# Kernel tuning notes

Hardware: AMD Instinct MI355X
Metric: run time of the kernel (lower is better)

## Reference

```python
import jax, jax.numpy as jnp
import numpy as np

PAD_ID = 0


def setup_inputs() -> dict:
    key = jax.random.key(0)
    ks = jax.random.split(key, 14)
    B, S, T = 64, 128, 32
    E = H = 512
    V = 32000
    s = 0.02
    return {
        "trg_tokens": jax.random.randint(ks[0], (B, T), 0, V),
        "src_tokens": jax.random.randint(ks[1], (B, S), 0, V),
        "encoder_out": jax.random.normal(ks[2], (S, B, 2 * H), jnp.float32),
        "hidden": jax.random.normal(ks[3], (B, H), jnp.float32),
        "embed_w": jax.random.normal(ks[4], (V, E), jnp.float32) * s,
        "attn_W": jax.random.normal(ks[5], (H, 2 * H + H), jnp.float32) * s,
        "attn_b": jnp.zeros((H,), jnp.float32),
        "v": jax.random.uniform(ks[6], (H,), jnp.float32),
        "W_ih": jax.random.normal(ks[7], (3 * H, 2 * H + E), jnp.float32) * s,
        "W_hh": jax.random.normal(ks[8], (3 * H, H), jnp.float32) * s,
        "b_ih": jnp.zeros((3 * H,), jnp.float32),
        "b_hh": jnp.zeros((3 * H,), jnp.float32),
        "out_W": jax.random.normal(ks[9], (V, 2 * H + H + E), jnp.float32) * s,
        "out_b": jnp.zeros((V,), jnp.float32),
    }


def reference(trg_tokens, src_tokens, encoder_out, hidden, embed_w, attn_W,
              attn_b, v, W_ih, W_hh, b_ih, b_hh, out_W, out_b):
    # trg_tokens: [B, T], src_tokens: [B, S] (transposed inside, as in torch)
    B, T = trg_tokens.shape
    S = src_tokens.shape[1]
    H = hidden.shape[1]
    V = out_W.shape[0]

    # Embedding with padding_idx -> zero row at PAD_ID
    emb = embed_w.at[PAD_ID].set(0.0)
    mask = (src_tokens != PAD_ID)              # [B, S]
    enc_bt = jnp.transpose(encoder_out, (1, 0, 2))  # [B, S, 2H]
    trg = trg_tokens.T                          # [T, B]

    def step(h, tok):
        x = emb[tok]                            # [B, E]
        # Bahdanau attention
        hrep = jnp.broadcast_to(h[:, None, :], (B, S, H))
        feat = jnp.concatenate([hrep, enc_bt], axis=2)      # [B, S, H+2H]
        energy = jnp.tanh(feat @ attn_W.T + attn_b)          # [B, S, H]
        scores = jnp.einsum('bsd,d->bs', energy, v)          # [B, S]
        scores = jnp.where(mask, scores, -jnp.inf)
        attn = jax.nn.softmax(scores, axis=1)                # [B, S]
        weighted = jnp.einsum('bs,bsd->bd', attn, enc_bt)    # [B, 2H]
        # GRU cell (torch gate order: r, z, n)
        rnn_in = jnp.concatenate([x, weighted], axis=1)      # [B, E+2H]
        gi = rnn_in @ W_ih.T + b_ih                          # [B, 3H]
        gh = h @ W_hh.T + b_hh                               # [B, 3H]
        i_r, i_z, i_n = jnp.split(gi, 3, axis=1)
        h_r, h_z, h_n = jnp.split(gh, 3, axis=1)
        r = jax.nn.sigmoid(i_r + h_r)
        z = jax.nn.sigmoid(i_z + h_z)
        n = jnp.tanh(i_n + r * h_n)
        h_new = (1.0 - z) * n + z * h                        # [B, H]
        # Output projection over cat(output, weighted, x)
        out_feat = jnp.concatenate([h_new, weighted, x], axis=1)  # [B, 2H+H+E]
        logits = out_feat @ out_W.T + out_b                  # [B, V]
        return h_new, logits

    # Teacher forcing ratio = 1.0: inputs are trg[0:T-1]; outputs[0] stays zero
    _, logits_seq = jax.lax.scan(step, hidden, trg[:T - 1])  # [T-1, B, V]
    outputs = jnp.concatenate(
        [jnp.zeros((1, B, V), logits_seq.dtype), logits_seq], axis=0)
    return outputs
```

## Files before the change

kernel.cpp:

```cpp
#include <hip/hip_runtime.h>

typedef __attribute__((ext_vector_type(4))) float f32x4;
typedef __attribute__((ext_vector_type(2))) float f32x2;
typedef __attribute__((ext_vector_type(8))) short s16x8;
typedef __attribute__((ext_vector_type(4))) short s16x4;

#define B_ 64
#define S_ 128
#define T_ 32
#define H_ 512
#define V_ 32000
#define NTILES 2000

#define SY_TILE 32
#define SY_SLOT 64

__device__ __forceinline__ unsigned short f2bf(float f) {
  union { float f; unsigned u; } x; x.f = f;
  unsigned r = x.u + 0x7FFFu + ((x.u >> 16) & 1u);
  return (unsigned short)(r >> 16);
}
__device__ __forceinline__ float bf2f(unsigned short u) {
  union { unsigned u; float f; } x; x.u = ((unsigned)u) << 16; return x.f;
}
__device__ __forceinline__ float fast_tanh(float x) {
  float e = __expf(2.0f * x);
  return 1.0f - 2.0f / (e + 1.0f);
}
__device__ __forceinline__ float fast_sig(float x) {
  return 1.0f / (1.0f + __expf(-x));
}
__device__ __forceinline__ void gload16(const void* g, void* l) {
  __builtin_amdgcn_global_load_lds(
      (const __attribute__((address_space(1))) void*)g,
      (__attribute__((address_space(3))) void*)l, 16, 0, 0);
}
__device__ __forceinline__ void gload16nt(const void* g, void* l) {
  __builtin_amdgcn_global_load_lds(
      (const __attribute__((address_space(1))) void*)g,
      (__attribute__((address_space(3))) void*)l, 16, 0, 2);
}

__device__ __forceinline__ unsigned ald(const unsigned* p) {
  return __hip_atomic_load(p, __ATOMIC_RELAXED, __HIP_MEMORY_SCOPE_AGENT);
}
__device__ __forceinline__ void ast(unsigned* p, unsigned v) {
  __hip_atomic_store(p, v, __ATOMIC_RELAXED, __HIP_MEMORY_SCOPE_AGENT);
}
__device__ __forceinline__ void astf(float* p, float v) {
  union { unsigned u; float f; } x; x.f = v; ast((unsigned*)p, x.u);
}

__device__ __forceinline__ void phase_sync(unsigned* sync, int bid,
                                           unsigned st_ph, int nmask,
                                           unsigned wt_ph) {
  __syncthreads();
  if (threadIdx.x == 0)
    __hip_atomic_store(&sync[SY_SLOT + bid], st_ph, __ATOMIC_RELEASE,
                       __HIP_MEMORY_SCOPE_AGENT);
  if (threadIdx.x < 64) {
    const unsigned* p = &sync[SY_SLOT + (threadIdx.x & nmask)];
    while (ald(p) < wt_ph) __builtin_amdgcn_s_sleep(1);
  }
  __syncthreads();
}

template <int OUTBF>
__global__ __launch_bounds__(256) void big_gemm_k(
    const unsigned short* __restrict__ A, int lda,
    const unsigned short* __restrict__ W, const float* __restrict__ bias,
    void* __restrict__ Cv, int Mv, int N, int K) {
  __shared__ unsigned short As[128 * 32];
  __shared__ unsigned short Bs[128 * 32];
  const int t = threadIdx.x;
  const int wave = t >> 6, lane = t & 63;
  const int m0 = blockIdx.x * 128, n0 = blockIdx.y * 128;
  const int wm = (wave & 1) * 64, wn = (wave >> 1) * 64;
  const int fr = lane & 15, fq = lane >> 4;

  f32x4 acc[4][4];
#pragma unroll
  for (int i = 0; i < 4; ++i)
#pragma unroll
    for (int j = 0; j < 4; ++j) acc[i][j] = (f32x4){0.f, 0.f, 0.f, 0.f};

  const int g = (((lane & 3) ^ ((lane >> 3) & 3))) * 8;
  const size_t a_g0 = (size_t)(m0 + wave * 32 + (lane >> 2)) * lda + g;
  const size_t b_g0 = (size_t)(n0 + wave * 32 + (lane >> 2)) * K + g;
  unsigned short* As_w = As + wave * 1024;
  unsigned short* Bs_w = Bs + wave * 1024;
  const int sl = (fq ^ ((fr >> 1) & 3)) * 8;

  for (int kk = 0; kk < K; kk += 32) {
    gload16(A + a_g0 + kk, As_w);
    gload16(A + a_g0 + (size_t)16 * lda + kk, As_w + 512);
    gload16(W + b_g0 + kk, Bs_w);
    gload16(W + b_g0 + (size_t)16 * K + kk, Bs_w + 512);
    __syncthreads();
    s16x8 af[4], bfr[4];
#pragma unroll
    for (int f = 0; f < 4; ++f) {
      af[f] = *(const s16x8*)(As + (wm + f * 16 + fr) * 32 + sl);
      bfr[f] = *(const s16x8*)(Bs + (wn + f * 16 + fr) * 32 + sl);
    }
#pragma unroll
    for (int fm = 0; fm < 4; ++fm)
#pragma unroll
      for (int fn = 0; fn < 4; ++fn)
        acc[fm][fn] = __builtin_amdgcn_mfma_f32_16x16x32_bf16(af[fm], bfr[fn],
                                                              acc[fm][fn], 0, 0, 0);
    __syncthreads();
  }

#pragma unroll
  for (int fn = 0; fn < 4; ++fn) {
    int col = n0 + wn + fn * 16 + fr;
    float bv = bias[col];
#pragma unroll
    for (int fm = 0; fm < 4; ++fm) {
      int rb = m0 + wm + fm * 16 + fq * 4;
#pragma unroll
      for (int i = 0; i < 4; ++i) {
        int r = rb + i;
        if (r < Mv) {
          if (OUTBF)
            ((unsigned short*)Cv)[(size_t)r * N + col] = f2bf(acc[fm][fn][i] + bv);
          else
            ((float*)Cv)[(size_t)r * N + col] = acc[fm][fn][i] + bv;
        }
      }
    }
  }
}

__global__ __launch_bounds__(512) void fused_k(
    float* __restrict__ h, unsigned short* __restrict__ hbf_step,
    float* __restrict__ hgh_step, const unsigned short* __restrict__ Wcomb,
    const unsigned short* __restrict__ encp_bf,
    const unsigned short* __restrict__ enc_bf, const float* __restrict__ v,
    const int* __restrict__ src_tok, const unsigned short* __restrict__ Ww,
    const unsigned short* __restrict__ gix, const float* __restrict__ b_hh,
    unsigned short* __restrict__ Abf, const unsigned short* __restrict__ outW,
    const float* __restrict__ out_b, float* __restrict__ out,
    unsigned* __restrict__ sync) {
  __shared__ __align__(16) char smem[62464];
  __shared__ unsigned sh_idx;
  const int t = threadIdx.x;
  const int lane = t & 63, w = t >> 6;
  const int fr = lane & 15, fq = lane >> 4;

  if (blockIdx.x < 64) {
    unsigned short* Asm = (unsigned short*)smem;
    unsigned short* Wsm = (unsigned short*)(smem + 9216);
    unsigned short* Wp1 = (unsigned short*)(smem + 16128);
    float* gsm = (float*)(smem + 49408);
    float* sc = (float*)(smem + 61696);
    const int j = blockIdx.x;
    const int ar = t >> 3, ak = (t & 7) * 8;
    const int p1_n0 = j * 32;
    const int rowt_p1 = w & 3, colt_p1 = w >> 2;

#pragma unroll
    for (int c = 0; c < 4; ++c) {
      int id = t * 4 + c;
      int r = id >> 6, cc = id & 63;
      s16x8 wv = *(const s16x8*)(Wcomb + (size_t)(p1_n0 + r) * 512 + cc * 8);
      *(s16x8*)(Wp1 + r * 520 + cc * 8) = wv;
    }
    __syncthreads();

    for (int step = 0; step < 31; ++step) {
      const unsigned short* hbfS = hbf_step + (size_t)step * 64 * 512;
      unsigned short* hbfS1 = hbf_step + (size_t)(step + 1) * 64 * 512;
      float* hghS = hgh_step + (size_t)step * 64 * 2048;
      const unsigned ph = 3u * step;

      {
        s16x8 pa[8];
#pragma unroll
        for (int p = 0; p < 8; ++p)
          pa[p] = *(const s16x8*)(hbfS + ar * 512 + p * 64 + ak);
        f32x4 acc = {0.f, 0.f, 0.f, 0.f};
#pragma unroll
        for (int it = 0; it < 8; ++it) {
          *(s16x8*)(Asm + ar * 72 + ak) = pa[it];
          __syncthreads();
          s16x8 a0 = *(const s16x8*)(Asm + (rowt_p1 * 16 + fr) * 72 + fq * 8);
          s16x8 a1 = *(const s16x8*)(Asm + (rowt_p1 * 16 + fr) * 72 + 32 + fq * 8);
          s16x8 b0 =
              *(const s16x8*)(Wp1 + (colt_p1 * 16 + fr) * 520 + it * 64 + fq * 8);
          s16x8 b1 = *(const s16x8*)(Wp1 + (colt_p1 * 16 + fr) * 520 + it * 64 +
                                     32 + fq * 8);
          acc = __builtin_amdgcn_mfma_f32_16x16x32_bf16(a0, b0, acc, 0, 0, 0);
          acc = __builtin_amdgcn_mfma_f32_16x16x32_bf16(a1, b1, acc, 0, 0, 0);
          __syncthreads();
        }
        int col = p1_n0 + colt_p1 * 16 + fr;
#pragma unroll
        for (int i = 0; i < 4; ++i)
          astf(&hghS[(rowt_p1 * 16 + fq * 4 + i) * 2048 + col], acc[i]);
      }
      phase_sync(sync, j, ph + 1, 15, ph + 1);

      {
        const int b = j;
        const float* hp = hghS + (size_t)b * 2048;
        float vh[8], hh[8];
        {
          f32x4 v0 = *(const f32x4*)(v + lane * 8);
          f32x4 v1 = *(const f32x4*)(v + lane * 8 + 4);
          f32x4 h0 = *(const f32x4*)(hp + lane * 8);
          f32x4 h1 = *(const f32x4*)(hp + lane * 8 + 4);
#pragma unroll
          for (int q = 0; q < 4; ++q) {
            vh[q] = v0[q]; vh[4 + q] = v1[q];
            hh[q] = h0[q]; hh[4 + q] = h1[q];
          }
        }
        for (int s = w * 16; s < w * 16 + 16; ++s) {
          s16x8 e =
              *(const s16x8*)(encp_bf + (size_t)(b * 128 + s) * 512 + lane * 8);
          float p = 0.f;
#pragma unroll
          for (int q = 0; q < 8; ++q)
            p += vh[q] * fast_tanh(hh[q] + bf2f((unsigned short)e[q]));
          for (int m = 32; m; m >>= 1) p += __shfl_xor(p, m);
          if (lane == 0)
            sc[s] = (src_tok[b * 128 + s] != 0) ? p : -__builtin_inff();
        }
        __syncthreads();
        if (t < 64) {
          float a0 = sc[t], a1 = sc[t + 64];
          float mx = fmaxf(a0, a1);
          for (int m = 32; m; m >>= 1) mx = fmaxf(mx, __shfl_xor(mx, m));
          float e0 = __expf(a0 - mx), e1 = __expf(a1 - mx);
          float ssum = e0 + e1;
          for (int m = 32; m; m >>= 1) ssum += __shfl_xor(ssum, m);
          float inv = 1.0f / ssum;
          sc[t] = e0 * inv;
          sc[t + 64] = e1 * inv;
        }
        __syncthreads();
        const int d = t * 2;
        float w0 = 0.f, w1 = 0.f;
#pragma unroll 16
        for (int s = 0; s < 128; ++s) {
          float a = sc[s];
          unsigned u = *(const unsigned*)(enc_bf + (size_t)(b * 128 + s) * 1024 + d);
          union { unsigned u; float f; } lo, hi;
          lo.u = u << 16; hi.u = u & 0xffff0000u;
          w0 += a * lo.f; w1 += a * hi.f;
        }
        unsigned pk = ((unsigned)f2bf(w1) << 16) | (unsigned)f2bf(w0);
        ast((unsigned*)(Abf + (size_t)(step * 64 + b) * 2048 + 512 + d), pk);
      }
      phase_sync(sync, j, ph + 2, 63, ph + 2);

      if (j < 32) {
        const int d0 = j * 16;
        const int r0 = step * 64;
        const int rowt = (w < 4) ? w : (w - 4);
        const int wgate = ar >> 4, wdr = ar & 15;
        const unsigned short* wwrow =
            Ww + (size_t)(wgate * 512 + d0 + wdr) * 1024 + ak;
        const unsigned short* abrow = Abf + (size_t)(r0 + ar) * 2048 + 512 + ak;
        s16x8 pa[8], pw[8];
#pragma unroll
        for (int p = 0; p < 8; ++p) {
          pa[p] = *(const s16x8*)(abrow + p * 64);
          if (t < 384) pw[p] = *(const s16x8*)(wwrow + p * 64);
        }
        f32x4 acc0 = {0.f, 0.f, 0.f, 0.f}, acc1 = {0.f, 0.f, 0.f, 0.f};
#pragma unroll
        for (int it = 0; it < 16; ++it) {
          *(s16x8*)(Asm + ar * 72 + ak) = pa[it & 7];
          if (t < 384) *(s16x8*)(Wsm + ar * 72 + ak) = pw[it & 7];
          __syncthreads();
          if (it < 8) {
            pa[it] = *(const s16x8*)(abrow + (it + 8) * 64);
            if (t < 384) pw[it] = *(const s16x8*)(wwrow + (it + 8) * 64);
          }
          s16x8 a0 = *(const s16x8*)(Asm + (rowt * 16 + fr) * 72 + fq * 8);
          s16x8 a1 = *(const s16x8*)(Asm + (rowt * 16 + fr) * 72 + 32 + fq * 8);
          if (w < 4) {
            s16x8 b0 = *(const s16x8*)(Wsm + fr * 72 + fq * 8);
            s16x8 b1 = *(const s16x8*)(Wsm + fr * 72 + 32 + fq * 8);
            s16x8 c0 = *(const s16x8*)(Wsm + (32 + fr) * 72 + fq * 8);
            s16x8 c1 = *(const s16x8*)(Wsm + (32 + fr) * 72 + 32 + fq * 8);
            acc0 = __builtin_amdgcn_mfma_f32_16x16x32_bf16(a0, b0, acc0, 0, 0, 0);
            acc0 = __builtin_amdgcn_mfma_f32_16x16x32_bf16(a1, b1, acc0, 0, 0, 0);
            acc1 = __builtin_amdgcn_mfma_f32_16x16x32_bf16(a0, c0, acc1, 0, 0, 0);
            acc1 = __builtin_amdgcn_mfma_f32_16x16x32_bf16(a1, c1, acc1, 0, 0, 0);
          } else {
            s16x8 b0 = *(const s16x8*)(Wsm + (16 + fr) * 72 + fq * 8);
            s16x8 b1 = *(const s16x8*)(Wsm + (16 + fr) * 72 + 32 + fq * 8);
            acc0 = __builtin_amdgcn_mfma_f32_16x16x32_bf16(a0, b0, acc0, 0, 0, 0);
            acc0 = __builtin_amdgcn_mfma_f32_16x16x32_bf16(a1, b1, acc0, 0, 0, 0);
          }
          __syncthreads();
        }
        {
          const int colt0 = (w < 4) ? 0 : 1;
#pragma unroll
          for (int i = 0; i < 4; ++i) {
            int row = rowt * 16 + fq * 4 + i;
            gsm[row * 48 + colt0 * 16 + fr] =
                acc0[i] +
                bf2f(gix[(size_t)(r0 + row) * 1536 + colt0 * 512 + d0 + fr]);
          }
          if (w < 4) {
#pragma unroll
            for (int i = 0; i < 4; ++i) {
              int row = rowt * 16 + fq * 4 + i;
              gsm[row * 48 + 32 + fr] =
                  acc1[i] + bf2f(gix[(size_t)(r0 + row) * 1536 + 1024 + d0 + fr]);
            }
          }
        }
        __syncthreads();
        {
          int e = t * 2;
          int b = e >> 4, dd = e & 15, d = d0 + dd;
          float hv2[2];
          unsigned short hb2[2];
#pragma unroll
          for (int k = 0; k < 2; ++k) {
            float ir = gsm[b * 48 + dd + k];
            float iz = gsm[b * 48 + 16 + dd + k];
            float inn = gsm[b * 48 + 32 + dd + k];
            float hr = hghS[b * 2048 + 512 + d + k] + b_hh[d + k];
            float hz = hghS[b * 2048 + 1024 + d + k] + b_hh[512 + d + k];
            float hn = hghS[b * 2048 + 1536 + d + k] + b_hh[1024 + d + k];
            float r = fast_sig(ir + hr);
            float z = fast_sig(iz + hz);
            float n = fast_tanh(inn + r * hn);
            hv2[k] = (1.0f - z) * n + z * h[b * 512 + d + k];
            hb2[k] = f2bf(hv2[k]);
          }
          h[b * 512 + d] = hv2[0];
          h[b * 512 + d + 1] = hv2[1];
          unsigned pk = ((unsigned)hb2[1] << 16) | (unsigned)hb2[0];
          ast((unsigned*)(hbfS1 + b * 512 + d), pk);
          ast((unsigned*)(Abf + (size_t)(r0 + b) * 2048 + d), pk);
        }
      }
      phase_sync(sync, j, ph + 3, 31, ph + 3);
    }
  }

  unsigned short* As2 = (unsigned short*)smem;
  unsigned short* Bs2 = (unsigned short*)(smem + 16384);
  const int wr = (w >> 2) * 64, wc = (w & 3) * 64;

  int rowA[2], cgA[2], rowB[4], cgB[4];
#pragma unroll
  for (int c = 0; c < 2; ++c) {
    int id = (w * 2 + c) * 64 + lane;
    rowA[c] = id >> 3;
    cgA[c] = ((id & 7) - rowA[c]) & 7;
  }
#pragma unroll
  for (int c = 0; c < 4; ++c) {
    int id = (w * 4 + c) * 64 + lane;
    rowB[c] = id >> 3;
    cgB[c] = ((id & 7) - rowB[c]) & 7;
  }

  for (;;) {
    __syncthreads();
    if (t == 0)
      sh_idx = __hip_atomic_fetch_add(&sync[SY_TILE], 1u, __ATOMIC_RELAXED,
                                      __HIP_MEMORY_SCOPE_AGENT);
    __syncthreads();
    unsigned idx = sh_idx;
    if (idx >= NTILES) break;
    int mb = idx / 125;
    int nt = idx - mb * 125;
    int gate = mb * 2 + 1;
    if (gate > 30) gate = 30;
    unsigned need = 3u * gate + 3u;
    if (w == 0) {
      const unsigned* p = &sync[SY_SLOT + (lane & 31)];
      while (ald(p) < need) __builtin_amdgcn_s_sleep(16);
    }
    __syncthreads();

    const int m0 = mb * 128, n0 = nt * 256;
    f32x4 acc[4][4];
#pragma unroll
    for (int i = 0; i < 4; ++i)
#pragma unroll
      for (int jj = 0; jj < 4; ++jj) acc[i][jj] = (f32x4){0.f, 0.f, 0.f, 0.f};

    for (int kk = 0; kk < 2048; kk += 64) {
#pragma unroll
      for (int c = 0; c < 2; ++c)
        gload16(Abf + (size_t)(m0 + rowA[c]) * 2048 + kk + cgA[c] * 8,
                As2 + (w * 2 + c) * 512);
#pragma unroll
      for (int c = 0; c < 4; ++c)
        gload16nt(outW + (size_t)(n0 + rowB[c]) * 2048 + kk + cgB[c] * 8,
                  Bs2 + (w * 4 + c) * 512);
      __syncthreads();
#pragma unroll
      for (int kh = 0; kh < 2; ++kh) {
        int cg = kh * 4 + fq;
        s16x8 af[4], bf_[4];
#pragma unroll
        for (int i = 0; i < 4; ++i) {
          int row = wr + i * 16 + fr;
          af[i] = *(const s16x8*)(As2 + row * 64 + (((cg + row) & 7) * 8));
        }
#pragma unroll
        for (int jj = 0; jj < 4; ++jj) {
          int row = wc + jj * 16 + fr;
          bf_[jj] = *(const s16x8*)(Bs2 + row * 64 + (((cg + row) & 7) * 8));
        }
#pragma unroll
        for (int i = 0; i < 4; ++i)
#pragma unroll
          for (int jj = 0; jj < 4; ++jj)
            acc[i][jj] = __builtin_amdgcn_mfma_f32_16x16x32_bf16(
                af[i], bf_[jj], acc[i][jj], 0, 0, 0);
      }
      __syncthreads();
    }

#pragma unroll
    for (int jj = 0; jj < 4; ++jj) {
      int col = n0 + wc + jj * 16 + fr;
      float bv = out_b[col];
#pragma unroll
      for (int i = 0; i < 4; ++i) {
        int rb = m0 + wr + i * 16 + fq * 4;
#pragma unroll
        for (int ii = 0; ii < 4; ++ii) {
          int r = rb + ii;
          if (r < 1984) out[(size_t)(r + 64) * V_ + col] = acc[i][jj][ii] + bv;
        }
      }
    }
  }
}

__global__ __launch_bounds__(256) void cast_bf16_k(const float* __restrict__ src,
                                                   unsigned short* __restrict__ dst,
                                                   int n4) {
  int i = blockIdx.x * 256 + threadIdx.x;
  if (i >= n4) return;
  f32x4 f = *(const f32x4*)(src + (size_t)i * 4);
  s16x4 o;
#pragma unroll
  for (int q = 0; q < 4; ++q) o[q] = (short)f2bf(f[q]);
  *(s16x4*)(dst + (size_t)i * 4) = o;
}

__global__ __launch_bounds__(256) void enc_cast_k(const float* __restrict__ enc,
                                                  unsigned short* __restrict__ dst) {
  int i = blockIdx.x * 256 + threadIdx.x;
  int n = i * 4;
  int row = n >> 10, d = n & 1023;
  int s = row & (S_ - 1), b = row >> 7;
  f32x4 f = *(const f32x4*)(enc + ((size_t)s * B_ + b) * 1024 + d);
  s16x4 o;
#pragma unroll
  for (int q = 0; q < 4; ++q) o[q] = (short)f2bf(f[q]);
  *(s16x4*)(dst + (size_t)row * 1024 + d) = o;
}

__global__ __launch_bounds__(256) void build_wcomb_k(const float* __restrict__ aW,
                                                     const float* __restrict__ whh,
                                                     unsigned short* __restrict__ dst) {
  int idx = (blockIdx.x * 256 + threadIdx.x) * 4;
  int n = idx >> 9, k = idx & 511;
  const float* src = (n < 512) ? (aW + (size_t)n * 1536 + k)
                               : (whh + (size_t)(n - 512) * 512 + k);
  f32x4 f = *(const f32x4*)src;
  s16x4 o;
#pragma unroll
  for (int q = 0; q < 4; ++q) o[q] = (short)f2bf(f[q]);
  *(s16x4*)(dst + idx) = o;
}

__global__ __launch_bounds__(256) void build_wenc_k(const float* __restrict__ aW,
                                                    unsigned short* __restrict__ dst) {
  int idx = (blockIdx.x * 256 + threadIdx.x) * 4;
  int n = idx >> 10, k = idx & 1023;
  f32x4 f = *(const f32x4*)(aW + (size_t)n * 1536 + 512 + k);
  s16x4 o;
#pragma unroll
  for (int q = 0; q < 4; ++q) o[q] = (short)f2bf(f[q]);
  *(s16x4*)(dst + idx) = o;
}

__global__ __launch_bounds__(256) void build_wxw_k(const float* __restrict__ wih,
                                                   unsigned short* __restrict__ wx,
                                                   unsigned short* __restrict__ ww) {
  int flat = blockIdx.x * 256 + threadIdx.x;
  int n = flat / 384, c4 = (flat % 384) * 4;
  f32x4 f = *(const f32x4*)(wih + (size_t)n * 1536 + c4);
  s16x4 o;
#pragma unroll
  for (int q = 0; q < 4; ++q) o[q] = (short)f2bf(f[q]);
  if (c4 < 512)
    *(s16x4*)(wx + (size_t)n * 512 + c4) = o;
  else
    *(s16x4*)(ww + (size_t)n * 1024 + (c4 - 512)) = o;
}

__global__ __launch_bounds__(256) void hcast_k(const float* __restrict__ hidden,
                                               unsigned short* __restrict__ hbf0) {
  int i = blockIdx.x * 256 + threadIdx.x;
  f32x2 f = *(const f32x2*)(hidden + (size_t)i * 2);
  unsigned pk = ((unsigned)f2bf(f[1]) << 16) | (unsigned)f2bf(f[0]);
  *(unsigned*)(hbf0 + (size_t)i * 2) = pk;
}

__global__ __launch_bounds__(256) void xgather_k(const int* __restrict__ trg,
                                                 const float* __restrict__ embed,
                                                 unsigned short* __restrict__ Abf) {
  int row = blockIdx.x;
  int tt = row >> 6, b = row & 63;
  int tok = trg[b * T_ + tt];
  int d = threadIdx.x * 2;
  unsigned pk = 0;
  if (tok != 0) {
    f32x2 f = *(const f32x2*)(embed + (size_t)tok * H_ + d);
    pk = ((unsigned)f2bf(f[1]) << 16) | (unsigned)f2bf(f[0]);
  }
  *(unsigned*)(Abf + (size_t)row * 2048 + 1536 + d) = pk;
}

extern "C" void kernel_launch(void* const* d_in, const int* in_sizes, int n_in,
                              void* d_out, int out_size, void* d_ws, size_t ws_size,
                              hipStream_t stream) {
  const int* trg = (const int*)d_in[0];
  const int* srt = (const int*)d_in[1];
  const float* enc = (const float*)d_in[2];
  const float* hidden = (const float*)d_in[3];
  const float* embed = (const float*)d_in[4];
  const float* attn_W = (const float*)d_in[5];
  const float* attn_b = (const float*)d_in[6];
  const float* vv = (const float*)d_in[7];
  const float* W_ih = (const float*)d_in[8];
  const float* W_hh = (const float*)d_in[9];
  const float* b_ih = (const float*)d_in[10];
  const float* b_hh = (const float*)d_in[11];
  const float* out_W = (const float*)d_in[12];
  const float* out_b = (const float*)d_in[13];
  float* out = (float*)d_out;

  char* ws = (char*)d_ws;
  size_t off = 0;
  auto alloc = [&](size_t bytes) {
    size_t o = off;
    off += (bytes + 255) & ~(size_t)255;
    return ws + o;
  };

  unsigned short* outW_bf = (unsigned short*)alloc((size_t)V_ * 2048 * 2);
  unsigned short* Abf = (unsigned short*)alloc((size_t)2048 * 2048 * 2);
  unsigned short* enc_bf = (unsigned short*)alloc((size_t)B_ * S_ * 1024 * 2);
  unsigned short* encp_bf = (unsigned short*)alloc((size_t)B_ * S_ * 512 * 2);
  unsigned short* gix_bf = (unsigned short*)alloc((size_t)1984 * 1536 * 2);
  unsigned short* Wcomb = (unsigned short*)alloc((size_t)2048 * 512 * 2);
  unsigned short* Wenc = (unsigned short*)alloc((size_t)512 * 1024 * 2);
  unsigned short* Wx = (unsigned short*)alloc((size_t)1536 * 512 * 2);
  unsigned short* Ww = (unsigned short*)alloc((size_t)1536 * 1024 * 2);
  float* hgh_step = (float*)alloc((size_t)31 * B_ * 2048 * 4);
  unsigned short* hbf_step = (unsigned short*)alloc((size_t)32 * B_ * H_ * 2);
  float* h = (float*)alloc((size_t)B_ * H_ * 4);
  unsigned* syncb = (unsigned*)alloc(8192);

  hipMemsetAsync(out, 0, (size_t)B_ * V_ * 4, stream);
  hipMemsetAsync(syncb, 0, 8192, stream);
  hipMemsetAsync(Abf + (size_t)1984 * 2048, 0, (size_t)64 * 2048 * 2, stream);
  hipMemcpyAsync(h, hidden, (size_t)B_ * H_ * 4, hipMemcpyDeviceToDevice, stream);

  cast_bf16_k<<<(V_ * 2048 / 4 + 255) / 256, 256, 0, stream>>>(out_W, outW_bf,
                                                               V_ * 2048 / 4);
  build_wcomb_k<<<2048 * 512 / 4 / 256, 256, 0, stream>>>(attn_W, W_hh, Wcomb);
  build_wenc_k<<<512 * 1024 / 4 / 256, 256, 0, stream>>>(attn_W, Wenc);
  build_wxw_k<<<1536 * 384 / 256, 256, 0, stream>>>(W_ih, Wx, Ww);
  hcast_k<<<64, 256, 0, stream>>>(hidden, hbf_step);
  enc_cast_k<<<B_ * S_ * 1024 / 4 / 256, 256, 0, stream>>>(enc, enc_bf);
  xgather_k<<<1984, 256, 0, stream>>>(trg, embed, Abf);

  big_gemm_k<1><<<dim3(64, 4), 256, 0, stream>>>(enc_bf, 1024, Wenc, attn_b,
                                                 encp_bf, B_ * S_, 512, 1024);
  big_gemm_k<1><<<dim3(16, 12), 256, 0, stream>>>(Abf + 1536, 2048, Wx, b_ih,
                                                  gix_bf, 1984, 1536, 512);

  fused_k<<<256, 512, 0, stream>>>(h, hbf_step, hgh_step, Wcomb, encp_bf, enc_bf,
                                   vv, srt, Ww, gix_bf, b_hh, Abf, outW_bf, out_b,
                                   out, syncb);
}
```

Measured before the change: 1.715 ms.

## Precompute encoder×W_ih projection so attention-weighted gates fuse into attention blocks

Uses linearity to precompute enc @ Ww^T for every source position (encp2), so each per-batch attention block builds its GRU input gates as an attention-weighted sum of projected rows instead of running a separate per-step GEMM. This removes one grid-wide phase barrier per step, and the GRU update runs in the same block with the hidden state kept in a register. The encoder cast kernel is dropped and the encoder GEMMs read fp32 input directly. In exchange it adds a large precomputed tensor (B*S*1536 bf16) that every step must stream, and the weighted sum over the gate inputs is rounded differently.

```diff
diff --git a/kernel.cpp b/kernel.cpp
--- a/kernel.cpp
+++ b/kernel.cpp
@@ -52,14 +52,13 @@
 }
 
 __device__ __forceinline__ void phase_sync(unsigned* sync, int bid,
-                                           unsigned st_ph, int nmask,
-                                           unsigned wt_ph) {
+                                           unsigned st_ph, unsigned wt_ph) {
   __syncthreads();
   if (threadIdx.x == 0)
     __hip_atomic_store(&sync[SY_SLOT + bid], st_ph, __ATOMIC_RELEASE,
                        __HIP_MEMORY_SCOPE_AGENT);
   if (threadIdx.x < 64) {
-    const unsigned* p = &sync[SY_SLOT + (threadIdx.x & nmask)];
+    const unsigned* p = &sync[SY_SLOT + threadIdx.x];
     while (ald(p) < wt_ph) __builtin_amdgcn_s_sleep(1);
   }
   __syncthreads();
@@ -133,17 +132,91 @@
   }
 }
 
+__global__ __launch_bounds__(256) void gemm_enc_k(
+    const float* __restrict__ A, const unsigned short* __restrict__ W,
+    const float* __restrict__ bias, unsigned short* __restrict__ C, int N) {
+  const int K = 1024;
+  __shared__ unsigned short As[128 * 32];
+  __shared__ unsigned short Bs[128 * 32];
+  const int t = threadIdx.x;
+  const int wave = t >> 6, lane = t & 63;
+  const int m0 = blockIdx.x * 128, n0 = blockIdx.y * 128;
+  const int wm = (wave & 1) * 64, wn = (wave >> 1) * 64;
+  const int fr = lane & 15, fq = lane >> 4;
+
+  f32x4 acc[4][4];
+#pragma unroll
+  for (int i = 0; i < 4; ++i)
+#pragma unroll
+    for (int j = 0; j < 4; ++j) acc[i][j] = (f32x4){0.f, 0.f, 0.f, 0.f};
+
+  const int g = (((lane & 3) ^ ((lane >> 3) & 3))) * 8;
+  const size_t b_g0 = (size_t)(n0 + wave * 32 + (lane >> 2)) * K + g;
+  unsigned short* Bs_w = Bs + wave * 1024;
+  const int sl = (fq ^ ((fr >> 1) & 3)) * 8;
+
+  const int r = t >> 1, gc0 = (t & 1) * 2;
+  const int m = m0 + r;
+  const float* arow = A + ((size_t)(m & 127) * 64 + (m >> 7)) * 1024;
+  const int c0 = (gc0 ^ ((r >> 1) & 3));
+  const int c1 = ((gc0 + 1) ^ ((r >> 1) & 3));
+
+  for (int kk = 0; kk < K; kk += 32) {
+    f32x4 a0 = *(const f32x4*)(arow + kk + gc0 * 8);
+    f32x4 a1 = *(const f32x4*)(arow + kk + gc0 * 8 + 4);
+    f32x4 a2 = *(const f32x4*)(arow + kk + gc0 * 8 + 8);
+    f32x4 a3 = *(const f32x4*)(arow + kk + gc0 * 8 + 12);
+    gload16(W + b_g0 + kk, Bs_w);
+    gload16(W + b_g0 + (size_t)16 * K + kk, Bs_w + 512);
+    s16x8 v0, v1;
+#pragma unroll
+    for (int q = 0; q < 4; ++q) {
+      v0[q] = (short)f2bf(a0[q]); v0[4 + q] = (short)f2bf(a1[q]);
+      v1[q] = (short)f2bf(a2[q]); v1[4 + q] = (short)f2bf(a3[q]);
+    }
+    *(s16x8*)(As + r * 32 + c0 * 8) = v0;
+    *(s16x8*)(As + r * 32 + c1 * 8) = v1;
+    __syncthreads();
+    s16x8 af[4], bfr[4];
+#pragma unroll
+    for (int f = 0; f < 4; ++f) {
+      af[f] = *(const s16x8*)(As + (wm + f * 16 + fr) * 32 + sl);
+      bfr[f] = *(const s16x8*)(Bs + (wn + f * 16 + fr) * 32 + sl);
+    }
+#pragma unroll
+    for (int fm = 0; fm < 4; ++fm)
+#pragma unroll
+      for (int fn = 0; fn < 4; ++fn)
+        acc[fm][fn] = __builtin_amdgcn_mfma_f32_16x16x32_bf16(af[fm], bfr[fn],
+                                                              acc[fm][fn], 0, 0, 0);
+    __syncthreads();
+  }
+
+#pragma unroll
+  for (int fn = 0; fn < 4; ++fn) {
+    int col = n0 + wn + fn * 16 + fr;
+    float bv = bias[col];
+#pragma unroll
+    for (int fm = 0; fm < 4; ++fm) {
+      int rb = m0 + wm + fm * 16 + fq * 4;
+#pragma unroll
+      for (int i = 0; i < 4; ++i)
+        C[(size_t)(rb + i) * N + col] = f2bf(acc[fm][fn][i] + bv);
+    }
+  }
+}
+
 __global__ __launch_bounds__(512) void fused_k(
-    float* __restrict__ h, unsigned short* __restrict__ hbf_step,
+    const float* __restrict__ hidden, unsigned short* __restrict__ hbf_step,
     float* __restrict__ hgh_step, const unsigned short* __restrict__ Wcomb,
     const unsigned short* __restrict__ encp_bf,
-    const unsigned short* __restrict__ enc_bf, const float* __restrict__ v,
-    const int* __restrict__ src_tok, const unsigned short* __restrict__ Ww,
-    const unsigned short* __restrict__ gix, const float* __restrict__ b_hh,
-    unsigned short* __restrict__ Abf, const unsigned short* __restrict__ outW,
-    const float* __restrict__ out_b, float* __restrict__ out,
-    unsigned* __restrict__ sync) {
-  __shared__ __align__(16) char smem[62464];
+    const unsigned short* __restrict__ encp2,
+    const float* __restrict__ enc, const float* __restrict__ v,
+    const int* __restrict__ src_tok, const unsigned short* __restrict__ gix,
+    const float* __restrict__ b_hh, unsigned short* __restrict__ Abf,
+    const unsigned short* __restrict__ outW, const float* __restrict__ out_b,
+    float* __restrict__ out, unsigned* __restrict__ sync) {
+  __shared__ __align__(16) char smem[49408];
   __shared__ unsigned sh_idx;
   const int t = threadIdx.x;
   const int lane = t & 63, w = t >> 6;
@@ -151,14 +224,15 @@
 
   if (blockIdx.x < 64) {
     unsigned short* Asm = (unsigned short*)smem;
-    unsigned short* Wsm = (unsigned short*)(smem + 9216);
-    unsigned short* Wp1 = (unsigned short*)(smem + 16128);
-    float* gsm = (float*)(smem + 49408);
-    float* sc = (float*)(smem + 61696);
+    unsigned short* Wp1 = (unsigned short*)(smem + 9216);
+    float* gsm = (float*)(smem + 42496);
+    float* sc = (float*)(smem + 48640);
     const int j = blockIdx.x;
     const int ar = t >> 3, ak = (t & 7) * 8;
     const int p1_n0 = j * 32;
     const int rowt_p1 = w & 3, colt_p1 = w >> 2;
+
+    float h_reg = hidden[(size_t)j * 512 + t];
 
 #pragma unroll
     for (int c = 0; c < 4; ++c) {
@@ -173,7 +247,7 @@
       const unsigned short* hbfS = hbf_step + (size_t)step * 64 * 512;
       unsigned short* hbfS1 = hbf_step + (size_t)(step + 1) * 64 * 512;
       float* hghS = hgh_step + (size_t)step * 64 * 2048;
-      const unsigned ph = 3u * step;
+      const unsigned ph = 2u * step;
 
       {
         s16x8 pa[8];
@@ -200,7 +274,7 @@
         for (int i = 0; i < 4; ++i)
           astf(&hghS[(rowt_p1 * 16 + fq * 4 + i) * 2048 + col], acc[i]);
       }
-      phase_sync(sync, j, ph + 1, 15, ph + 1);
+      phase_sync(sync, j, ph + 1, ph + 1);
 
       {
         const int b = j;
@@ -241,110 +315,53 @@
           sc[t + 64] = e1 * inv;
         }
         __syncthreads();
+
         const int d = t * 2;
+        const int kk = t * 4;
         float w0 = 0.f, w1 = 0.f;
-#pragma unroll 16
+        f32x4 g4 = {0.f, 0.f, 0.f, 0.f};
+#pragma unroll 8
         for (int s = 0; s < 128; ++s) {
           float a = sc[s];
-          unsigned u = *(const unsigned*)(enc_bf + (size_t)(b * 128 + s) * 1024 + d);
-          union { unsigned u; float f; } lo, hi;
-          lo.u = u << 16; hi.u = u & 0xffff0000u;
-          w0 += a * lo.f; w1 += a * hi.f;
-        }
-        unsigned pk = ((unsigned)f2bf(w1) << 16) | (unsigned)f2bf(w0);
-        ast((unsigned*)(Abf + (size_t)(step * 64 + b) * 2048 + 512 + d), pk);
+          f32x2 e = *(const f32x2*)(enc + ((size_t)s * 64 + b) * 1024 + d);
+          w0 += a * e[0]; w1 += a * e[1];
+          if (t < 384) {
+            s16x4 p2 = *(const s16x4*)(encp2 + (size_t)(b * 128 + s) * 1536 + kk);
+            g4[0] += a * bf2f((unsigned short)p2[0]);
+            g4[1] += a * bf2f((unsigned short)p2[1]);
+            g4[2] += a * bf2f((unsigned short)p2[2]);
+            g4[3] += a * bf2f((unsigned short)p2[3]);
+          }
+        }
+        const int row = step * 64 + b;
+        unsigned pkw = ((unsigned)f2bf(w1) << 16) | (unsigned)f2bf(w0);
+        ast((unsigned*)(Abf + (size_t)row * 2048 + 512 + d), pkw);
+        if (t < 384) *(f32x4*)(gsm + kk) = g4;
+        __syncthreads();
+
+        {
+          const unsigned short* gr = gix + (size_t)row * 1536;
+          float ir = gsm[t] + bf2f(gr[t]);
+          float iz = gsm[512 + t] + bf2f(gr[512 + t]);
+          float inn = gsm[1024 + t] + bf2f(gr[1024 + t]);
+          float hr = hghS[b * 2048 + 512 + t] + b_hh[t];
+          float hz = hghS[b * 2048 + 1024 + t] + b_hh[512 + t];
+          float hn = hghS[b * 2048 + 1536 + t] + b_hh[1024 + t];
+          float r = fast_sig(ir + hr);
+          float z = fast_sig(iz + hz);
+          float n = fast_tanh(inn + r * hn);
+          float hv = (1.0f - z) * n + z * h_reg;
+          h_reg = hv;
+          unsigned hb = (unsigned)f2bf(hv);
+          unsigned other = (unsigned)__shfl_xor((int)hb, 1);
+          if ((t & 1) == 0) {
+            unsigned pk = (other << 16) | hb;
+            ast((unsigned*)(hbfS1 + (size_t)b * 512 + t), pk);
+            ast((unsigned*)(Abf + (size_t)row * 2048 + t), pk);
+          }
+        }
       }
-      phase_sync(sync, j, ph + 2, 63, ph + 2);
-
-      if (j < 32) {
-        const int d0 = j * 16;
-        const int r0 = step * 64;
-        const int rowt = (w < 4) ? w : (w - 4);
-        const int wgate = ar >> 4, wdr = ar & 15;
-        const unsigned short* wwrow =
-            Ww + (size_t)(wgate * 512 + d0 + wdr) * 1024 + ak;
-        const unsigned short* abrow = Abf + (size_t)(r0 + ar) * 2048 + 512 + ak;
-        s16x8 pa[8], pw[8];
-#pragma unroll
-        for (int p = 0; p < 8; ++p) {
-          pa[p] = *(const s16x8*)(abrow + p * 64);
-          if (t < 384) pw[p] = *(const s16x8*)(wwrow + p * 64);
-        }
-        f32x4 acc0 = {0.f, 0.f, 0.f, 0.f}, acc1 = {0.f, 0.f, 0.f, 0.f};
-#pragma unroll
-        for (int it = 0; it < 16; ++it) {
-          *(s16x8*)(Asm + ar * 72 + ak) = pa[it & 7];
-          if (t < 384) *(s16x8*)(Wsm + ar * 72 + ak) = pw[it & 7];
-          __syncthreads();
-          if (it < 8) {
-            pa[it] = *(const s16x8*)(abrow + (it + 8) * 64);
-            if (t < 384) pw[it] = *(const s16x8*)(wwrow + (it + 8) * 64);
-          }
-          s16x8 a0 = *(const s16x8*)(Asm + (rowt * 16 + fr) * 72 + fq * 8);
-          s16x8 a1 = *(const s16x8*)(Asm + (rowt * 16 + fr) * 72 + 32 + fq * 8);
-          if (w < 4) {
-            s16x8 b0 = *(const s16x8*)(Wsm + fr * 72 + fq * 8);
-            s16x8 b1 = *(const s16x8*)(Wsm + fr * 72 + 32 + fq * 8);
-            s16x8 c0 = *(const s16x8*)(Wsm + (32 + fr) * 72 + fq * 8);
-            s16x8 c1 = *(const s16x8*)(Wsm + (32 + fr) * 72 + 32 + fq * 8);
-            acc0 = __builtin_amdgcn_mfma_f32_16x16x32_bf16(a0, b0, acc0, 0, 0, 0);
-            acc0 = __builtin_amdgcn_mfma_f32_16x16x32_bf16(a1, b1, acc0, 0, 0, 0);
-            acc1 = __builtin_amdgcn_mfma_f32_16x16x32_bf16(a0, c0, acc1, 0, 0, 0);
-            acc1 = __builtin_amdgcn_mfma_f32_16x16x32_bf16(a1, c1, acc1, 0, 0, 0);
-          } else {
-            s16x8 b0 = *(const s16x8*)(Wsm + (16 + fr) * 72 + fq * 8);
-            s16x8 b1 = *(const s16x8*)(Wsm + (16 + fr) * 72 + 32 + fq * 8);
-            acc0 = __builtin_amdgcn_mfma_f32_16x16x32_bf16(a0, b0, acc0, 0, 0, 0);
-            acc0 = __builtin_amdgcn_mfma_f32_16x16x32_bf16(a1, b1, acc0, 0, 0, 0);
-          }
-          __syncthreads();
-        }
-        {
-          const int colt0 = (w < 4) ? 0 : 1;
-#pragma unroll
-          for (int i = 0; i < 4; ++i) {
-            int row = rowt * 16 + fq * 4 + i;
-            gsm[row * 48 + colt0 * 16 + fr] =
-                acc0[i] +
-                bf2f(gix[(size_t)(r0 + row) * 1536 + colt0 * 512 + d0 + fr]);
-          }
-          if (w < 4) {
-#pragma unroll
-            for (int i = 0; i < 4; ++i) {
-              int row = rowt * 16 + fq * 4 + i;
-              gsm[row * 48 + 32 + fr] =
-                  acc1[i] + bf2f(gix[(size_t)(r0 + row) * 1536 + 1024 + d0 + fr]);
-            }
-          }
-        }
-        __syncthreads();
-        {
-          int e = t * 2;
-          int b = e >> 4, dd = e & 15, d = d0 + dd;
-          float hv2[2];
-          unsigned short hb2[2];
-#pragma unroll
-          for (int k = 0; k < 2; ++k) {
-            float ir = gsm[b * 48 + dd + k];
-            float iz = gsm[b * 48 + 16 + dd + k];
-            float inn = gsm[b * 48 + 32 + dd + k];
-            float hr = hghS[b * 2048 + 512 + d + k] + b_hh[d + k];
-            float hz = hghS[b * 2048 + 1024 + d + k] + b_hh[512 + d + k];
-            float hn = hghS[b * 2048 + 1536 + d + k] + b_hh[1024 + d + k];
-            float r = fast_sig(ir + hr);
-            float z = fast_sig(iz + hz);
-            float n = fast_tanh(inn + r * hn);
-            hv2[k] = (1.0f - z) * n + z * h[b * 512 + d + k];
-            hb2[k] = f2bf(hv2[k]);
-          }
-          h[b * 512 + d] = hv2[0];
-          h[b * 512 + d + 1] = hv2[1];
-          unsigned pk = ((unsigned)hb2[1] << 16) | (unsigned)hb2[0];
-          ast((unsigned*)(hbfS1 + b * 512 + d), pk);
-          ast((unsigned*)(Abf + (size_t)(r0 + b) * 2048 + d), pk);
-        }
-      }
-      phase_sync(sync, j, ph + 3, 31, ph + 3);
+      phase_sync(sync, j, ph + 2, ph + 2);
     }
   }
 
@@ -378,9 +395,9 @@
     int nt = idx - mb * 125;
     int gate = mb * 2 + 1;
     if (gate > 30) gate = 30;
-    unsigned need = 3u * gate + 3u;
+    unsigned need = 2u * gate + 2u;
     if (w == 0) {
-      const unsigned* p = &sync[SY_SLOT + (lane & 31)];
+      const unsigned* p = &sync[SY_SLOT + lane];
       while (ald(p) < need) __builtin_amdgcn_s_sleep(16);
     }
     __syncthreads();
@@ -408,13 +425,13 @@
         s16x8 af[4], bf_[4];
 #pragma unroll
         for (int i = 0; i < 4; ++i) {
-          int row = wr + i * 16 + fr;
-          af[i] = *(const s16x8*)(As2 + row * 64 + (((cg + row) & 7) * 8));
+          int rr = wr + i * 16 + fr;
+          af[i] = *(const s16x8*)(As2 + rr * 64 + (((cg + rr) & 7) * 8));
         }
 #pragma unroll
         for (int jj = 0; jj < 4; ++jj) {
-          int row = wc + jj * 16 + fr;
-          bf_[jj] = *(const s16x8*)(Bs2 + row * 64 + (((cg + row) & 7) * 8));
+          int rr = wc + jj * 16 + fr;
+          bf_[jj] = *(const s16x8*)(Bs2 + rr * 64 + (((cg + rr) & 7) * 8));
         }
 #pragma unroll
         for (int i = 0; i < 4; ++i)
@@ -453,19 +470,6 @@
 #pragma unroll
   for (int q = 0; q < 4; ++q) o[q] = (short)f2bf(f[q]);
   *(s16x4*)(dst + (size_t)i * 4) = o;
-}
-
-__global__ __launch_bounds__(256) void enc_cast_k(const float* __restrict__ enc,
-                                                  unsigned short* __restrict__ dst) {
-  int i = blockIdx.x * 256 + threadIdx.x;
-  int n = i * 4;
-  int row = n >> 10, d = n & 1023;
-  int s = row & (S_ - 1), b = row >> 7;
-  f32x4 f = *(const f32x4*)(enc + ((size_t)s * B_ + b) * 1024 + d);
-  s16x4 o;
-#pragma unroll
-  for (int q = 0; q < 4; ++q) o[q] = (short)f2bf(f[q]);
-  *(s16x4*)(dst + (size_t)row * 1024 + d) = o;
 }
 
 __global__ __launch_bounds__(256) void build_wcomb_k(const float* __restrict__ aW,
@@ -560,8 +564,8 @@
 
   unsigned short* outW_bf = (unsigned short*)alloc((size_t)V_ * 2048 * 2);
   unsigned short* Abf = (unsigned short*)alloc((size_t)2048 * 2048 * 2);
-  unsigned short* enc_bf = (unsigned short*)alloc((size_t)B_ * S_ * 1024 * 2);
   unsigned short* encp_bf = (unsigned short*)alloc((size_t)B_ * S_ * 512 * 2);
+  unsigned short* encp2 = (unsigned short*)alloc((size_t)B_ * S_ * 1536 * 2);
   unsigned short* gix_bf = (unsigned short*)alloc((size_t)1984 * 1536 * 2);
   unsigned short* Wcomb = (unsigned short*)alloc((size_t)2048 * 512 * 2);
   unsigned short* Wenc = (unsigned short*)alloc((size_t)512 * 1024 * 2);
@@ -569,13 +573,13 @@
   unsigned short* Ww = (unsigned short*)alloc((size_t)1536 * 1024 * 2);
   float* hgh_step = (float*)alloc((size_t)31 * B_ * 2048 * 4);
   unsigned short* hbf_step = (unsigned short*)alloc((size_t)32 * B_ * H_ * 2);
-  float* h = (float*)alloc((size_t)B_ * H_ * 4);
+  float* zbias = (float*)alloc(2048 * 4);
   unsigned* syncb = (unsigned*)alloc(8192);
 
   hipMemsetAsync(out, 0, (size_t)B_ * V_ * 4, stream);
   hipMemsetAsync(syncb, 0, 8192, stream);
+  hipMemsetAsync(zbias, 0, 2048 * 4, stream);
   hipMemsetAsync(Abf + (size_t)1984 * 2048, 0, (size_t)64 * 2048 * 2, stream);
-  hipMemcpyAsync(h, hidden, (size_t)B_ * H_ * 4, hipMemcpyDeviceToDevice, stream);
 
   cast_bf16_k<<<(V_ * 2048 / 4 + 255) / 256, 256, 0, stream>>>(out_W, outW_bf,
                                                                V_ * 2048 / 4);
@@ -583,15 +587,14 @@
   build_wenc_k<<<512 * 1024 / 4 / 256, 256, 0, stream>>>(attn_W, Wenc);
   build_wxw_k<<<1536 * 384 / 256, 256, 0, stream>>>(W_ih, Wx, Ww);
   hcast_k<<<64, 256, 0, stream>>>(hidden, hbf_step);
-  enc_cast_k<<<B_ * S_ * 1024 / 4 / 256, 256, 0, stream>>>(enc, enc_bf);
   xgather_k<<<1984, 256, 0, stream>>>(trg, embed, Abf);
 
-  big_gemm_k<1><<<dim3(64, 4), 256, 0, stream>>>(enc_bf, 1024, Wenc, attn_b,
-                                                 encp_bf, B_ * S_, 512, 1024);
+  gemm_enc_k<<<dim3(64, 4), 256, 0, stream>>>(enc, Wenc, attn_b, encp_bf, 512);
+  gemm_enc_k<<<dim3(64, 12), 256, 0, stream>>>(enc, Ww, zbias, encp2, 1536);
   big_gemm_k<1><<<dim3(16, 12), 256, 0, stream>>>(Abf + 1536, 2048, Wx, b_ih,
                                                   gix_bf, 1984, 1536, 512);
 
-  fused_k<<<256, 512, 0, stream>>>(h, hbf_step, hgh_step, Wcomb, encp_bf, enc_bf,
-                                   vv, srt, Ww, gix_bf, b_hh, Abf, outW_bf, out_b,
-                                   out, syncb);
-}
+  fused_k<<<256, 512, 0, stream>>>(hidden, hbf_step, hgh_step, Wcomb, encp_bf,
+                                   encp2, enc, vv, srt, gix_bf, b_hh, Abf,
+                                   outW_bf, out_b, out, syncb);
+}
```

New measurement: 2.505 ms. 46.1% more time.
